# Kernel optimization log

Measured on AMD Instinct MI355X. Metric: run time of the kernel, lower is better.

## Reference

```python
import jax, jax.numpy as jnp
import numpy as np

MD = 20          # max_displacement
TEMP = 1e-4      # softmax temperature
B, C, H, W = 4, 64, 112, 112


def setup_inputs() -> dict:
    key = jax.random.key(0)
    k1, k2 = jax.random.split(key)
    in1 = jax.random.normal(k1, (B, C, H, W), dtype=jnp.float32)
    in2 = jax.random.normal(k2, (B, C, H, W), dtype=jnp.float32)
    return {"in1": in1, "in2": in2}


def reference(in1, in2):
    b, c, h, w = in1.shape
    # F.normalize(x, dim=1): x / max(||x||_2, eps)
    def l2n(x):
        return x / jnp.maximum(jnp.linalg.norm(x, axis=1, keepdims=True), 1e-12)
    in1 = l2n(in1)
    in2 = l2n(in2)

    pad = jnp.pad(in2, ((0, 0), (0, 0), (MD, MD), (MD, MD)))

    d = jnp.arange(-MD, MD + 1)
    dx, dy = jnp.meshgrid(d, d, indexing="ij")  # torch.meshgrid default 'ij'
    dx = dx.reshape(-1)  # [K] with K = (2*MD+1)^2
    dy = dy.reshape(-1)

    def sim_one(dxi, dyi):
        # shifted window of padded in2, same spatial size as in1
        sl = jax.lax.dynamic_slice(pad, (0, 0, MD + dxi, MD + dyi), (b, c, h, w))
        return jnp.sum(in1 * sl, axis=1)  # [B,H,W]

    sim = jax.vmap(sim_one)(dx, dy)          # [K,B,H,W]
    sim = jnp.transpose(sim, (1, 0, 2, 3))   # [B,K,H,W] cost volume

    weights = jax.nn.softmax(sim / TEMP, axis=1)  # softmax over displacements
    guide = jnp.stack((dx, dy), axis=-1).astype(jnp.float32)  # [K,2]
    # flow[b,d,h,w] = sum_k weights[b,k,h,w] * guide[k,d]
    flow = jnp.einsum("bkhw,kd->bdhw", weights, guide)
    return flow
```

## Files before the change

kernel.cpp:

```cpp
#include <hip/hip_runtime.h>
#include <math.h>

#define BB 4
#define CC 64
#define HH 112
#define WW 112
#define MD 20
#define KD 41
#define SCALE 10000.0f
#define NPIX (BB*HH*WW)
#define NT 10
#define ROW2 (NT*2*2*64*8)
#define IN2S_BYTES ((size_t)BB*HH*ROW2*2)

typedef _Float16 half8   __attribute__((ext_vector_type(8)));
typedef float    f32x4   __attribute__((ext_vector_type(4)));
typedef unsigned short ushort8 __attribute__((ext_vector_type(8)));

static __device__ __forceinline__ unsigned short f2h_bits(float x) {
    _Float16 h = (_Float16)x;
    return __builtin_bit_cast(unsigned short, h);
}
static __device__ __forceinline__ float h2f(unsigned short s) {
    return (float)__builtin_bit_cast(_Float16, s);
}

__global__ __launch_bounds__(256) void prep_kernel(const float* __restrict__ in1,
                                                   const float* __restrict__ in2,
                                                   unsigned short* __restrict__ in2s,
                                                   float* __restrict__ inv1) {
    __shared__ float sinv2[WW];
    int bid = blockIdx.x;
    int b = bid / HH, h = bid % HH;
    int t = threadIdx.x;

    if (t < WW) {
        float s = 0.f;
        for (int c = 0; c < CC; ++c) {
            float x = in2[((b*CC + c)*HH + h)*WW + t];
            s += x*x;
        }
        sinv2[t] = 1.0f / fmaxf(sqrtf(s), 1e-12f);
    } else if (t >= 128 && t < 128 + WW) {
        int w = t - 128;
        float s = 0.f;
        for (int c = 0; c < CC; ++c) {
            float x = in1[((b*CC + c)*HH + h)*WW + w];
            s += x*x;
        }
        inv1[(b*HH + h)*WW + w] = 1.0f / fmaxf(sqrtf(s), 1e-12f);
    }
    __syncthreads();

    int wave = t >> 6, lane = t & 63;
    int n = lane & 15, q = lane >> 4;
    unsigned short* base = in2s + (size_t)(b*HH + h)*ROW2;
    for (int tsk = wave; tsk < NT*2; tsk += 4) {
        int tau = tsk >> 1, ks = tsk & 1;
        int p = 16*tau + n, col = p - MD;
        ushort8 hb = {0,0,0,0,0,0,0,0}, lb = {0,0,0,0,0,0,0,0};
        if (col >= 0 && col < WW) {
            float iv = sinv2[col];
            #pragma unroll
            for (int j = 0; j < 8; ++j) {
                int c = 32*ks + 8*q + j;
                float x = in2[((b*CC + c)*HH + h)*WW + col] * iv;
                unsigned short xh = f2h_bits(x);
                float r = (x - h2f(xh)) * 4096.0f;
                hb[j] = xh;
                lb[j] = f2h_bits(r);
            }
        }
        *(ushort8*)(base + (size_t)((tau*4 + ks*2 + 0)*64 + lane)*8) = hb;
        *(ushort8*)(base + (size_t)((tau*4 + ks*2 + 1)*64 + lane)*8) = lb;
    }
}

__global__ __launch_bounds__(64, 3) void corr_kernel(const float* __restrict__ in1,
                                                     const unsigned short* __restrict__ in2s,
                                                     const float* __restrict__ inv1,
                                                     float* __restrict__ out) {
    int gid = blockIdx.x;
    int wt  = gid / (BB*HH);
    int rem = gid % (BB*HH);
    int b = rem / HH, h = rem % HH;
    int lane = threadIdx.x;
    int n = lane & 15, q = lane >> 4;
    int m0 = 4*q;

    int wA = wt*16 + n;
    float i1 = inv1[(b*HH + h)*WW + wA];
    half8 aH[2], aL[2];
    #pragma unroll
    for (int ks = 0; ks < 2; ++ks) {
        #pragma unroll
        for (int j = 0; j < 8; ++j) {
            int c = 32*ks + 8*q + j;
            float x = in1[((b*CC + c)*HH + h)*WW + wA] * i1;
            _Float16 xh = (_Float16)x;
            aH[ks][j] = xh;
            aL[ks][j] = (_Float16)((x - (float)xh) * 4096.0f);
        }
    }

    float nm20[4]; bool v0[4], v2[4], v3[4];
    #pragma unroll
    for (int r = 0; r < 4; ++r) {
        int nm = n - (m0 + r);
        nm20[r] = (float)(nm - 20);
        v0[r] = (nm >= 0);
        v2[r] = (nm <= 8);
        v3[r] = (nm <= -8);
    }

    float sm[4], sl[4], ssx[4], ssy[4];
    #pragma unroll
    for (int r = 0; r < 4; ++r) { sm[r] = -3.0f; sl[r] = 0.f; ssx[r] = 0.f; ssy[r] = 0.f; }

    int dlo = max(0, MD - h);
    int dhi = min(KD, HH + MD - h);

    for (int dxi = dlo; dxi < dhi; ++dxi) {
        const unsigned short* rb = in2s + (size_t)(b*HH + (h + dxi - MD))*ROW2;
        f32x4 s[4];
        #pragma unroll
        for (int oi = 0; oi < 4; ++oi) {
            int tau = wt + oi;
            const half8* fp = (const half8*)(rb + (size_t)(tau*4*64 + lane)*8);
            half8 bH0 = fp[0];
            half8 bL0 = fp[64];
            half8 bH1 = fp[128];
            half8 bL1 = fp[192];
            f32x4 a0 = {0.f,0.f,0.f,0.f}, a1 = {0.f,0.f,0.f,0.f};
            a0 = __builtin_amdgcn_mfma_f32_16x16x32_f16(aH[0], bH0, a0, 0, 0, 0);
            a1 = __builtin_amdgcn_mfma_f32_16x16x32_f16(aH[0], bL0, a1, 0, 0, 0);
            a1 = __builtin_amdgcn_mfma_f32_16x16x32_f16(aL[0], bH0, a1, 0, 0, 0);
            a0 = __builtin_amdgcn_mfma_f32_16x16x32_f16(aH[1], bH1, a0, 0, 0, 0);
            a1 = __builtin_amdgcn_mfma_f32_16x16x32_f16(aH[1], bL1, a1, 0, 0, 0);
            a1 = __builtin_amdgcn_mfma_f32_16x16x32_f16(aL[1], bH1, a1, 0, 0, 0);
            s[oi] = a0 + a1 * (1.0f/4096.0f);
        }
        float dxf = (float)(dxi - MD);
        #pragma unroll
        for (int r = 0; r < 4; ++r) {
            float s0v = v0[r] ? s[0][r] : -3.0f;
            float s1v = s[1][r];
            float s2v = v2[r] ? s[2][r] : -3.0f;
            float s3v = v3[r] ? s[3][r] : -3.0f;
            float mn = fmaxf(fmaxf(sm[r], s0v), fmaxf(fmaxf(s1v, s2v), s3v));
            float er = __expf((sm[r] - mn)*SCALE);
            float e0 = __expf((s0v - mn)*SCALE);
            float e1 = __expf((s1v - mn)*SCALE);
            float e2 = __expf((s2v - mn)*SCALE);
            float e3 = __expf((s3v - mn)*SCALE);
            float sum = (e0 + e1) + (e2 + e3);
            float tt  = e1 + 2.f*e2 + 3.f*e3;
            sl[r]  = sl[r]*er + sum;
            ssx[r] = ssx[r]*er + dxf*sum;
            ssy[r] = ssy[r]*er + (16.f*tt + nm20[r]*sum);
            sm[r]  = mn;
        }
    }

    int nlo = dlo, nhi = KD - dhi;
    if (nlo + nhi > 0) {
        float sdx = 0.f;
        for (int d = 0; d < nlo; ++d)  sdx += (float)(d - MD);
        for (int d = dhi; d < KD; ++d) sdx += (float)(d - MD);
        float cnt = (float)((nlo + nhi)*KD);
        #pragma unroll
        for (int r = 0; r < 4; ++r) {
            float mn = fmaxf(sm[r], 0.f);
            float er = __expf((sm[r] - mn)*SCALE);
            float e0 = __expf((0.f - mn)*SCALE);
            sl[r]  = sl[r]*er + cnt*e0;
            ssx[r] = ssx[r]*er + (float)KD*sdx*e0;
            ssy[r] = ssy[r]*er;
            sm[r]  = mn;
        }
    }

    #pragma unroll
    for (int off = 1; off < 16; off <<= 1) {
        #pragma unroll
        for (int r = 0; r < 4; ++r) {
            float m2 = __shfl_xor(sm[r],  off);
            float l2 = __shfl_xor(sl[r],  off);
            float x2 = __shfl_xor(ssx[r], off);
            float y2 = __shfl_xor(ssy[r], off);
            float mn = fmaxf(sm[r], m2);
            float ea = __expf((sm[r] - mn)*SCALE);
            float eb = __expf((m2    - mn)*SCALE);
            sl[r]  = sl[r]*ea  + l2*eb;
            ssx[r] = ssx[r]*ea + x2*eb;
            ssy[r] = ssy[r]*ea + y2*eb;
            sm[r]  = mn;
        }
    }

    if (n == 0) {
        #pragma unroll
        for (int r = 0; r < 4; ++r) {
            int w = wt*16 + m0 + r;
            out[((b*2 + 0)*HH + h)*WW + w] = ssx[r] / sl[r];
            out[((b*2 + 1)*HH + h)*WW + w] = ssy[r] / sl[r];
        }
    }
}

extern "C" void kernel_launch(void* const* d_in, const int* in_sizes, int n_in,
                              void* d_out, int out_size, void* d_ws, size_t ws_size,
                              hipStream_t stream) {
    const float* in1 = (const float*)d_in[0];
    const float* in2 = (const float*)d_in[1];
    float* out = (float*)d_out;
    unsigned short* in2s = (unsigned short*)d_ws;
    float* inv1 = (float*)((char*)d_ws + IN2S_BYTES);

    prep_kernel<<<BB*HH, 256, 0, stream>>>(in1, in2, in2s, inv1);
    corr_kernel<<<7*BB*HH, 64, 0, stream>>>(in1, in2s, inv1, out);
}
```

Measured before the change: 187.9 us.

## Split displacement range across blocks, XCD-aware mapping, separate norm/pack kernels, exp2

Each correlation block now handles half of the vertical displacement range, doubling the grid, and writes partial online-softmax state (max, sum, weighted sums) that a new merge kernel combines. Block indices are remapped so each XCD works on one batch and half the rows, for L2 locality of the packed in2 rows. Preprocessing is split into a norm kernel and a separately parallelised pack kernel that uses an LDS tile. In the inner loop all B-fragment loads are hoisted ahead of the MFMAs, and exp is replaced with a raw exp2 using a prescaled constant. The costs are two extra launches and a global round trip for the partial state.

```diff
diff --git a/kernel.cpp b/kernel.cpp
--- a/kernel.cpp
+++ b/kernel.cpp
@@ -1,5 +1,4 @@
 #include <hip/hip_runtime.h>
-#include <math.h>
 
 #define BB 4
 #define CC 64
@@ -7,7 +6,7 @@
 #define WW 112
 #define MD 20
 #define KD 41
-#define SCALE 10000.0f
+#define S2 14426.950408f
 #define NPIX (BB*HH*WW)
 #define NT 10
 #define ROW2 (NT*2*2*64*8)
@@ -17,6 +16,9 @@
 typedef float    f32x4   __attribute__((ext_vector_type(4)));
 typedef unsigned short ushort8 __attribute__((ext_vector_type(8)));
 
+static __device__ __forceinline__ float ex2(float x) {
+    return __builtin_amdgcn_exp2f(x);
+}
 static __device__ __forceinline__ unsigned short f2h_bits(float x) {
     _Float16 h = (_Float16)x;
     return __builtin_bit_cast(unsigned short, h);
@@ -24,52 +26,67 @@
 static __device__ __forceinline__ float h2f(unsigned short s) {
     return (float)__builtin_bit_cast(_Float16, s);
 }
-
-__global__ __launch_bounds__(256) void prep_kernel(const float* __restrict__ in1,
+static __device__ __forceinline__ float fmax_f(float a, float b) { return a > b ? a : b; }
+
+__global__ __launch_bounds__(128) void norm_kernel(const float* __restrict__ in1,
                                                    const float* __restrict__ in2,
-                                                   unsigned short* __restrict__ in2s,
-                                                   float* __restrict__ inv1) {
-    __shared__ float sinv2[WW];
+                                                   float* __restrict__ inv1,
+                                                   float* __restrict__ inv2) {
     int bid = blockIdx.x;
-    int b = bid / HH, h = bid % HH;
+    int which = bid / (BB*HH);
+    int rem = bid % (BB*HH);
+    int b = rem / HH, h = rem % HH;
     int t = threadIdx.x;
-
-    if (t < WW) {
-        float s = 0.f;
-        for (int c = 0; c < CC; ++c) {
-            float x = in2[((b*CC + c)*HH + h)*WW + t];
-            s += x*x;
-        }
-        sinv2[t] = 1.0f / fmaxf(sqrtf(s), 1e-12f);
-    } else if (t >= 128 && t < 128 + WW) {
-        int w = t - 128;
-        float s = 0.f;
-        for (int c = 0; c < CC; ++c) {
-            float x = in1[((b*CC + c)*HH + h)*WW + w];
-            s += x*x;
-        }
-        inv1[(b*HH + h)*WW + w] = 1.0f / fmaxf(sqrtf(s), 1e-12f);
+    if (t >= WW) return;
+    const float* src = which ? in2 : in1;
+    float s = 0.f;
+    #pragma unroll
+    for (int c = 0; c < CC; ++c) {
+        float x = src[((b*CC + c)*HH + h)*WW + t];
+        s += x*x;
+    }
+    float inv = 1.0f / fmax_f(__builtin_sqrtf(s), 1e-12f);
+    (which ? inv2 : inv1)[(b*HH + h)*WW + t] = inv;
+}
+
+__global__ __launch_bounds__(64) void pack_kernel(const float* __restrict__ in2,
+                                                  const float* __restrict__ inv2,
+                                                  unsigned short* __restrict__ in2s) {
+    __shared__ float tile[CC][17];
+    int bid = blockIdx.x;
+    int tau = bid % NT;
+    int bh  = bid / NT;
+    int b = bh / HH, h = bh % HH;
+    int lane = threadIdx.x;
+    int n = lane & 15, q = lane >> 4;
+    int col0 = 16*tau - MD;
+
+    #pragma unroll
+    for (int it = 0; it < 4; ++it) {
+        int c  = it*16 + (lane >> 2);
+        int k0 = (lane & 3) * 4;
+        const float* src = &in2[((b*CC + c)*HH + h)*WW];
+        #pragma unroll
+        for (int u = 0; u < 4; ++u) {
+            int cw = col0 + k0 + u;
+            tile[c][k0 + u] = (cw >= 0 && cw < WW) ? src[cw] : 0.f;
+        }
     }
     __syncthreads();
 
-    int wave = t >> 6, lane = t & 63;
-    int n = lane & 15, q = lane >> 4;
+    int col = col0 + n;
+    float iv = (col >= 0 && col < WW) ? inv2[(b*HH + h)*WW + col] : 0.f;
     unsigned short* base = in2s + (size_t)(b*HH + h)*ROW2;
-    for (int tsk = wave; tsk < NT*2; tsk += 4) {
-        int tau = tsk >> 1, ks = tsk & 1;
-        int p = 16*tau + n, col = p - MD;
-        ushort8 hb = {0,0,0,0,0,0,0,0}, lb = {0,0,0,0,0,0,0,0};
-        if (col >= 0 && col < WW) {
-            float iv = sinv2[col];
-            #pragma unroll
-            for (int j = 0; j < 8; ++j) {
-                int c = 32*ks + 8*q + j;
-                float x = in2[((b*CC + c)*HH + h)*WW + col] * iv;
-                unsigned short xh = f2h_bits(x);
-                float r = (x - h2f(xh)) * 4096.0f;
-                hb[j] = xh;
-                lb[j] = f2h_bits(r);
-            }
+    #pragma unroll
+    for (int ks = 0; ks < 2; ++ks) {
+        ushort8 hb, lb;
+        #pragma unroll
+        for (int j = 0; j < 8; ++j) {
+            int c = 32*ks + 8*q + j;
+            float x = tile[c][n] * iv;
+            unsigned short xh = f2h_bits(x);
+            hb[j] = xh;
+            lb[j] = f2h_bits((x - h2f(xh)) * 4096.0f);
         }
         *(ushort8*)(base + (size_t)((tau*4 + ks*2 + 0)*64 + lane)*8) = hb;
         *(ushort8*)(base + (size_t)((tau*4 + ks*2 + 1)*64 + lane)*8) = lb;
@@ -79,11 +96,16 @@
 __global__ __launch_bounds__(64, 3) void corr_kernel(const float* __restrict__ in1,
                                                      const unsigned short* __restrict__ in2s,
                                                      const float* __restrict__ inv1,
-                                                     float* __restrict__ out) {
+                                                     float* __restrict__ part) {
     int gid = blockIdx.x;
-    int wt  = gid / (BB*HH);
-    int rem = gid % (BB*HH);
-    int b = rem / HH, h = rem % HH;
+    int xcd  = gid & 7;
+    int slot = gid >> 3;
+    int hloc = slot % 56;
+    int tmp  = slot / 56;
+    int dg = tmp & 1;
+    int wt = tmp >> 1;
+    int b  = xcd >> 1;
+    int h  = (xcd & 1)*56 + hloc;
     int lane = threadIdx.x;
     int n = lane & 15, q = lane >> 4;
     int m0 = 4*q;
@@ -117,27 +139,34 @@
     #pragma unroll
     for (int r = 0; r < 4; ++r) { sm[r] = -3.0f; sl[r] = 0.f; ssx[r] = 0.f; ssy[r] = 0.f; }
 
-    int dlo = max(0, MD - h);
-    int dhi = min(KD, HH + MD - h);
-
-    for (int dxi = dlo; dxi < dhi; ++dxi) {
+    int glo = dg ? 21 : 0;
+    int ghi = dg ? KD : 21;
+    int lo = glo > (MD - h) ? glo : (MD - h);
+    int hi0 = HH + MD - h;
+    int hi = ghi < hi0 ? ghi : hi0;
+    if (hi < lo) { lo = ghi; hi = ghi; }
+
+    for (int dxi = lo; dxi < hi; ++dxi) {
         const unsigned short* rb = in2s + (size_t)(b*HH + (h + dxi - MD))*ROW2;
+        half8 bf[4][4];
+        #pragma unroll
+        for (int oi = 0; oi < 4; ++oi) {
+            const half8* fp = (const half8*)(rb + (size_t)((wt+oi)*4*64 + lane)*8);
+            bf[oi][0] = fp[0];
+            bf[oi][1] = fp[64];
+            bf[oi][2] = fp[128];
+            bf[oi][3] = fp[192];
+        }
         f32x4 s[4];
         #pragma unroll
         for (int oi = 0; oi < 4; ++oi) {
-            int tau = wt + oi;
-            const half8* fp = (const half8*)(rb + (size_t)(tau*4*64 + lane)*8);
-            half8 bH0 = fp[0];
-            half8 bL0 = fp[64];
-            half8 bH1 = fp[128];
-            half8 bL1 = fp[192];
             f32x4 a0 = {0.f,0.f,0.f,0.f}, a1 = {0.f,0.f,0.f,0.f};
-            a0 = __builtin_amdgcn_mfma_f32_16x16x32_f16(aH[0], bH0, a0, 0, 0, 0);
-            a1 = __builtin_amdgcn_mfma_f32_16x16x32_f16(aH[0], bL0, a1, 0, 0, 0);
-            a1 = __builtin_amdgcn_mfma_f32_16x16x32_f16(aL[0], bH0, a1, 0, 0, 0);
-            a0 = __builtin_amdgcn_mfma_f32_16x16x32_f16(aH[1], bH1, a0, 0, 0, 0);
-            a1 = __builtin_amdgcn_mfma_f32_16x16x32_f16(aH[1], bL1, a1, 0, 0, 0);
-            a1 = __builtin_amdgcn_mfma_f32_16x16x32_f16(aL[1], bH1, a1, 0, 0, 0);
+            a0 = __builtin_amdgcn_mfma_f32_16x16x32_f16(aH[0], bf[oi][0], a0, 0, 0, 0);
+            a1 = __builtin_amdgcn_mfma_f32_16x16x32_f16(aH[0], bf[oi][1], a1, 0, 0, 0);
+            a1 = __builtin_amdgcn_mfma_f32_16x16x32_f16(aL[0], bf[oi][0], a1, 0, 0, 0);
+            a0 = __builtin_amdgcn_mfma_f32_16x16x32_f16(aH[1], bf[oi][2], a0, 0, 0, 0);
+            a1 = __builtin_amdgcn_mfma_f32_16x16x32_f16(aH[1], bf[oi][3], a1, 0, 0, 0);
+            a1 = __builtin_amdgcn_mfma_f32_16x16x32_f16(aL[1], bf[oi][2], a1, 0, 0, 0);
             s[oi] = a0 + a1 * (1.0f/4096.0f);
         }
         float dxf = (float)(dxi - MD);
@@ -147,12 +176,12 @@
             float s1v = s[1][r];
             float s2v = v2[r] ? s[2][r] : -3.0f;
             float s3v = v3[r] ? s[3][r] : -3.0f;
-            float mn = fmaxf(fmaxf(sm[r], s0v), fmaxf(fmaxf(s1v, s2v), s3v));
-            float er = __expf((sm[r] - mn)*SCALE);
-            float e0 = __expf((s0v - mn)*SCALE);
-            float e1 = __expf((s1v - mn)*SCALE);
-            float e2 = __expf((s2v - mn)*SCALE);
-            float e3 = __expf((s3v - mn)*SCALE);
+            float mn = fmax_f(fmax_f(sm[r], s0v), fmax_f(fmax_f(s1v, s2v), s3v));
+            float er = ex2((sm[r] - mn)*S2);
+            float e0 = ex2((s0v - mn)*S2);
+            float e1 = ex2((s1v - mn)*S2);
+            float e2 = ex2((s2v - mn)*S2);
+            float e3 = ex2((s3v - mn)*S2);
             float sum = (e0 + e1) + (e2 + e3);
             float tt  = e1 + 2.f*e2 + 3.f*e3;
             sl[r]  = sl[r]*er + sum;
@@ -162,17 +191,16 @@
         }
     }
 
-    int nlo = dlo, nhi = KD - dhi;
-    if (nlo + nhi > 0) {
-        float sdx = 0.f;
-        for (int d = 0; d < nlo; ++d)  sdx += (float)(d - MD);
-        for (int d = dhi; d < KD; ++d) sdx += (float)(d - MD);
-        float cnt = (float)((nlo + nhi)*KD);
-        #pragma unroll
-        for (int r = 0; r < 4; ++r) {
-            float mn = fmaxf(sm[r], 0.f);
-            float er = __expf((sm[r] - mn)*SCALE);
-            float e0 = __expf((0.f - mn)*SCALE);
+    int cnt_i = (lo - glo) + (ghi - hi);
+    if (cnt_i > 0) {
+        float sdx = (float)(lo - glo) * (0.5f*(float)(glo + lo - 1) - (float)MD)
+                  + (float)(ghi - hi) * (0.5f*(float)(ghi + hi - 1) - (float)MD);
+        float cnt = (float)cnt_i * (float)KD;
+        #pragma unroll
+        for (int r = 0; r < 4; ++r) {
+            float mn = fmax_f(sm[r], 0.f);
+            float er = ex2((sm[r] - mn)*S2);
+            float e0 = ex2((0.f - mn)*S2);
             sl[r]  = sl[r]*er + cnt*e0;
             ssx[r] = ssx[r]*er + (float)KD*sdx*e0;
             ssy[r] = ssy[r]*er;
@@ -188,9 +216,9 @@
             float l2 = __shfl_xor(sl[r],  off);
             float x2 = __shfl_xor(ssx[r], off);
             float y2 = __shfl_xor(ssy[r], off);
-            float mn = fmaxf(sm[r], m2);
-            float ea = __expf((sm[r] - mn)*SCALE);
-            float eb = __expf((m2    - mn)*SCALE);
+            float mn = fmax_f(sm[r], m2);
+            float ea = ex2((sm[r] - mn)*S2);
+            float eb = ex2((m2    - mn)*S2);
             sl[r]  = sl[r]*ea  + l2*eb;
             ssx[r] = ssx[r]*ea + x2*eb;
             ssy[r] = ssy[r]*ea + y2*eb;
@@ -202,10 +230,28 @@
         #pragma unroll
         for (int r = 0; r < 4; ++r) {
             int w = wt*16 + m0 + r;
-            out[((b*2 + 0)*HH + h)*WW + w] = ssx[r] / sl[r];
-            out[((b*2 + 1)*HH + h)*WW + w] = ssy[r] / sl[r];
-        }
-    }
+            int pix = (b*HH + h)*WW + w;
+            float* p = &part[(size_t)(dg*NPIX + pix)*4];
+            p[0] = sm[r]; p[1] = sl[r]; p[2] = ssx[r]; p[3] = ssy[r];
+        }
+    }
+}
+
+__global__ __launch_bounds__(256) void merge_kernel(const float* __restrict__ part,
+                                                    float* __restrict__ out) {
+    int idx = blockIdx.x*256 + threadIdx.x;
+    if (idx >= NPIX) return;
+    const float* p0 = &part[(size_t)idx*4];
+    const float* p1 = &part[(size_t)(NPIX + idx)*4];
+    float M = fmax_f(p0[0], p1[0]);
+    float e0 = ex2((p0[0] - M)*S2);
+    float e1 = ex2((p1[0] - M)*S2);
+    float L  = p0[1]*e0 + p1[1]*e1;
+    float SX = p0[2]*e0 + p1[2]*e1;
+    float SY = p0[3]*e0 + p1[3]*e1;
+    int b = idx / (HH*WW), rem = idx % (HH*WW);
+    out[(b*2 + 0)*(HH*WW) + rem] = SX / L;
+    out[(b*2 + 1)*(HH*WW) + rem] = SY / L;
 }
 
 extern "C" void kernel_launch(void* const* d_in, const int* in_sizes, int n_in,
@@ -216,7 +262,11 @@
     float* out = (float*)d_out;
     unsigned short* in2s = (unsigned short*)d_ws;
     float* inv1 = (float*)((char*)d_ws + IN2S_BYTES);
-
-    prep_kernel<<<BB*HH, 256, 0, stream>>>(in1, in2, in2s, inv1);
-    corr_kernel<<<7*BB*HH, 64, 0, stream>>>(in1, in2s, inv1, out);
-}
+    float* inv2 = inv1 + NPIX;
+    float* part = inv2 + NPIX;
+
+    norm_kernel <<<2*BB*HH, 128, 0, stream>>>(in1, in2, inv1, inv2);
+    pack_kernel <<<BB*HH*NT, 64, 0, stream>>>(in2, inv2, in2s);
+    corr_kernel <<<8*784, 64, 0, stream>>>(in1, in2s, inv1, part);
+    merge_kernel<<<(NPIX+255)/256, 256, 0, stream>>>(part, out);
+}
```

Measured after the change: 183.9 us. 1.02x faster.
